# Kernel tuning notes

Measured on AMD Instinct MI355X. Metric: run time of the kernel, lower is better.

Reference implementation:

```python
import jax, jax.numpy as jnp
import numpy as np

BS, L, D, N = 4, 2048, 1024, 16

def setup_inputs() -> dict:
    key = jax.random.key(0)
    ks = jax.random.split(key, 8)
    s = 1.0 / np.sqrt(D)
    x  = jax.random.normal(ks[0], (BS, L, D), dtype=jnp.float32)
    # torch Linear params; stored transposed so y = x @ W + b
    W1 = jax.random.uniform(ks[1], (D, D), jnp.float32, -s, s)
    b1 = jax.random.uniform(ks[2], (D,),   jnp.float32, -s, s)
    W2 = jax.random.uniform(ks[3], (D, N), jnp.float32, -s, s)
    b2 = jax.random.uniform(ks[4], (N,),   jnp.float32, -s, s)
    W3 = jax.random.uniform(ks[5], (D, N), jnp.float32, -s, s)
    b3 = jax.random.uniform(ks[6], (N,),   jnp.float32, -s, s)
    A  = jax.random.normal(ks[7], (D, N),  jnp.float32) * np.sqrt(2.0 / (D + N))  # xavier
    return {"x": x, "W1": W1, "b1": b1, "W2": W2, "b2": b2, "W3": W3, "b3": b3, "A": A}

def reference(x, W1, b1, W2, b2, W3, b3, A):
    # S6 forward (non-recurrent branch).
    B = x @ W2 + b2                     # (b,l,n)
    C = x @ W3 + b3                     # (b,l,n)
    delta = jax.nn.softplus(x @ W1 + b1)  # (b,l,d)
    # dA = exp(einsum('bld,dn->bldn', delta, A)) is multiplied by an all-zero h
    # in the original forward, so it does not affect the output (dead code under DCE).
    dB = jnp.einsum('bld,bln->bldn', delta, B)   # (b,l,d,n) -- 512 MB intermediate
    h = x[..., None] * dB                         # (b,l,d,n)
    y = jnp.einsum('bln,bldn->bld', C, h)         # (b,l,d)
    return y
```

## Files before the change

kernel.cpp:

```cpp
#include <hip/hip_runtime.h>
#include <hip/hip_bf16.h>
#include <math.h>


namespace {

constexpr int Dd   = 1024;
constexpr int ROWS = 8192;

typedef __bf16 bf16x8 __attribute__((ext_vector_type(8)));
typedef float  floatx4 __attribute__((ext_vector_type(4)));

__device__ __forceinline__ float softplus_fast(float v) {
    float l = __logf(1.0f + __expf(v));
    return v > 15.0f ? v : l;
}
__device__ __forceinline__ float bf_lo(unsigned short u) {
    union { unsigned q; float f; } c; c.q = ((unsigned)u) << 16; return c.f;
}

__device__ __forceinline__ void gld_lds16(const __bf16* g, __bf16* l) {
    __builtin_amdgcn_global_load_lds(
        (const __attribute__((address_space(1))) void*)g,
        (__attribute__((address_space(3))) void*)l, 16, 0, 0);
}

__global__ __launch_bounds__(256) void w23_kernel(
    const float* __restrict__ W2, const float* __restrict__ W3,
    __bf16* __restrict__ W2t, __bf16* __restrict__ W3t)
{
    const int t  = threadIdx.x;
    const int n  = t >> 4;
    const int k0 = blockIdx.x * 64 + (t & 15) * 4;
    ushort4 a, b;
    union { __bf16 h; unsigned short u; } c;
    c.h = (__bf16)W2[(size_t)(k0 + 0) * 16 + n]; a.x = c.u;
    c.h = (__bf16)W2[(size_t)(k0 + 1) * 16 + n]; a.y = c.u;
    c.h = (__bf16)W2[(size_t)(k0 + 2) * 16 + n]; a.z = c.u;
    c.h = (__bf16)W2[(size_t)(k0 + 3) * 16 + n]; a.w = c.u;
    c.h = (__bf16)W3[(size_t)(k0 + 0) * 16 + n]; b.x = c.u;
    c.h = (__bf16)W3[(size_t)(k0 + 1) * 16 + n]; b.y = c.u;
    c.h = (__bf16)W3[(size_t)(k0 + 2) * 16 + n]; b.z = c.u;
    c.h = (__bf16)W3[(size_t)(k0 + 3) * 16 + n]; b.w = c.u;
    *(ushort4*)&W2t[(size_t)n * Dd + k0] = a;
    *(ushort4*)&W3t[(size_t)n * Dd + k0] = b;
}

__global__ __launch_bounds__(256, 4) void prep_kernel(
    const float* __restrict__ X, const float* __restrict__ W1,
    const __bf16* __restrict__ W2t, const float* __restrict__ b2,
    const __bf16* __restrict__ W3t, const float* __restrict__ b3,
    __bf16* __restrict__ Xb, __bf16* __restrict__ W1t, float* __restrict__ Sv)
{
    const int t = threadIdx.x;

    if (blockIdx.x >= 512) {
        __shared__ __bf16 tile[64][66];
        const int bidx = blockIdx.x - 512;
        const int bi = bidx >> 4, bj = bidx & 15;
        const int c = t & 63, r4 = t >> 6;
        #pragma unroll
        for (int i = 0; i < 16; ++i) {
            const int r = i * 4 + r4;
            tile[r][c] = (__bf16)W1[(size_t)(bi * 64 + r) * Dd + bj * 64 + c];
        }
        __syncthreads();
        #pragma unroll
        for (int i = 0; i < 16; ++i) {
            const int r = i * 4 + r4;
            W1t[(size_t)(bj * 64 + r) * Dd + bi * 64 + c] = tile[c][r];
        }
        return;
    }

    __shared__ float red[4][2][16][16];
    const int w = t >> 6, lane = t & 63;
    const int l15 = lane & 15, quad = lane >> 4;
    const int row0 = blockIdx.x * 16;
    const int kw = w * 256;
    const size_t xoff = (size_t)(row0 + l15) * Dd;
    const size_t woff = (size_t)l15 * Dd;

    floatx4 acc0 = {0.f, 0.f, 0.f, 0.f}, acc1 = {0.f, 0.f, 0.f, 0.f};
    #pragma unroll
    for (int ks = 0; ks < 8; ++ks) {
        const int k0 = kw + ks * 32 + quad * 8;
        const float4 xa = *(const float4*)&X[xoff + k0];
        const float4 xb = *(const float4*)&X[xoff + k0 + 4];
        bf16x8 af;
        af[0] = (__bf16)xa.x; af[1] = (__bf16)xa.y;
        af[2] = (__bf16)xa.z; af[3] = (__bf16)xa.w;
        af[4] = (__bf16)xb.x; af[5] = (__bf16)xb.y;
        af[6] = (__bf16)xb.z; af[7] = (__bf16)xb.w;
        *(bf16x8*)&Xb[xoff + k0] = af;
        const bf16x8 w2f = *(const bf16x8*)&W2t[woff + k0];
        const bf16x8 w3f = *(const bf16x8*)&W3t[woff + k0];
        acc0 = __builtin_amdgcn_mfma_f32_16x16x32_bf16(af, w2f, acc0, 0, 0, 0);
        acc1 = __builtin_amdgcn_mfma_f32_16x16x32_bf16(af, w3f, acc1, 0, 0, 0);
    }
    #pragma unroll
    for (int r = 0; r < 4; ++r) {
        red[w][0][quad * 4 + r][l15] = acc0[r];
        red[w][1][quad * 4 + r][l15] = acc1[r];
    }
    __syncthreads();
    {
        const int r = t >> 4, n = t & 15;
        float B = b2[n], C = b3[n];
        #pragma unroll
        for (int ww = 0; ww < 4; ++ww) {
            B += red[ww][0][r][n];
            C += red[ww][1][r][n];
        }
        float p = B * C;
        p += __shfl_xor(p, 1); p += __shfl_xor(p, 2);
        p += __shfl_xor(p, 4); p += __shfl_xor(p, 8);
        if (n == 0) Sv[row0 + r] = p;
    }
}

__global__ __launch_bounds__(256, 2) void gemm_kernel(
    const __bf16* __restrict__ Xb, const __bf16* __restrict__ W1t,
    const float* __restrict__ Sv, const float* __restrict__ b1,
    float* __restrict__ Y)
{
    __shared__ __attribute__((aligned(16))) __bf16 lds[32768];
    const int t = threadIdx.x, lane = t & 63;
    const int w = t >> 6, wm = w & 1, wn = w >> 1;
    const int l15 = lane & 15, quad = lane >> 4;
    const int cb = blockIdx.x & 7, rb = blockIdx.x >> 3;
    const int row0 = rb * 128, col0 = cb * 128;

    floatx4 acc[4][4] = {};

    const __bf16* gA[4]; const __bf16* gB[4];
    int dA[4], dB[4];
    #pragma unroll
    for (int i = 0; i < 4; ++i) {
        const int u = i * 256 + t;
        const int r = u >> 3;
        const int c = (u & 7) ^ (r & 7);
        gA[i] = Xb  + (size_t)(row0 + r) * Dd + c * 8;
        gB[i] = W1t + (size_t)(col0 + r) * Dd + c * 8;
        dA[i] = u * 8;
        dB[i] = 16384 + u * 8;
    }

    auto stage = [&](int buf, int k) {
        #pragma unroll
        for (int i = 0; i < 4; ++i) {
            gld_lds16(gA[i] + k, &lds[buf * 8192 + dA[i]]);
            gld_lds16(gB[i] + k, &lds[buf * 8192 + dB[i]]);
        }
    };

    auto compute = [&](int buf) {
        const __bf16* Al = &lds[buf * 8192];
        const __bf16* Bl = &lds[16384 + buf * 8192];
        #pragma unroll
        for (int ks = 0; ks < 2; ++ks) {
            const int sA = ((ks << 2) | quad) ^ (l15 & 7);
            bf16x8 af[4], bfr[4];
            #pragma unroll
            for (int mt = 0; mt < 4; ++mt)
                af[mt] = *(const bf16x8*)&Al[(wm * 64 + mt * 16 + l15) * 64 + sA * 8];
            #pragma unroll
            for (int nt = 0; nt < 4; ++nt)
                bfr[nt] = *(const bf16x8*)&Bl[(wn * 64 + nt * 16 + l15) * 64 + sA * 8];
            #pragma unroll
            for (int mt = 0; mt < 4; ++mt)
                #pragma unroll
                for (int nt = 0; nt < 4; ++nt)
                    acc[mt][nt] = __builtin_amdgcn_mfma_f32_16x16x32_bf16(
                        af[mt], bfr[nt], acc[mt][nt], 0, 0, 0);
        }
    };

    stage(0, 0);
    #pragma unroll 1
    for (int k0 = 0; k0 < Dd - 64; k0 += 64) {
        const int cur = (k0 >> 6) & 1;
        stage(cur ^ 1, k0 + 64);
        asm volatile("s_waitcnt vmcnt(8)" ::: "memory");
        __builtin_amdgcn_s_barrier();
        compute(cur);
        asm volatile("s_waitcnt lgkmcnt(0)" ::: "memory");
        __builtin_amdgcn_s_barrier();
    }
    asm volatile("s_waitcnt vmcnt(0)" ::: "memory");
    __builtin_amdgcn_s_barrier();
    compute(((Dd >> 6) - 1) & 1);

    float bias[4];
    #pragma unroll
    for (int nt = 0; nt < 4; ++nt) bias[nt] = b1[col0 + wn * 64 + nt * 16 + l15];

    #pragma unroll
    for (int mt = 0; mt < 4; ++mt) {
        #pragma unroll
        for (int rr = 0; rr < 4; ++rr) {
            const int row = row0 + wm * 64 + mt * 16 + quad * 4 + rr;
            const float sv = Sv[row];
            const unsigned short* xrow =
                (const unsigned short*)(Xb + (size_t)row * Dd + col0);
            float* yrow = Y + (size_t)row * Dd + col0;
            #pragma unroll
            for (int nt = 0; nt < 4; ++nt) {
                const int cl = wn * 64 + nt * 16 + l15;
                const float v  = acc[mt][nt][rr] + bias[nt];
                const float sp = softplus_fast(v);
                yrow[cl] = bf_lo(xrow[cl]) * sp * sv;
            }
        }
    }
}

}

extern "C" void kernel_launch(void* const* d_in, const int* in_sizes, int n_in,
                              void* d_out, int out_size, void* d_ws, size_t ws_size,
                              hipStream_t stream)
{
    const float* X  = (const float*)d_in[0];
    const float* W1 = (const float*)d_in[1];
    const float* b1 = (const float*)d_in[2];
    const float* W2 = (const float*)d_in[3];
    const float* b2 = (const float*)d_in[4];
    const float* W3 = (const float*)d_in[5];
    const float* b3 = (const float*)d_in[6];
    float* Y = (float*)d_out;

    char* ws = (char*)d_ws;
    __bf16* Xb  = (__bf16*)ws;
    __bf16* W1t = (__bf16*)(ws + 16777216);
    float*  Sv  = (float*) (ws + 16777216 + 2097152);
    __bf16* W2t = (__bf16*)(ws + 16777216 + 2097152 + 32768);
    __bf16* W3t = (__bf16*)(ws + 16777216 + 2097152 + 65536);

    hipLaunchKernelGGL(w23_kernel, dim3(16), dim3(256), 0, stream, W2, W3, W2t, W3t);
    hipLaunchKernelGGL(prep_kernel, dim3(768), dim3(256), 0, stream,
                       X, W1, W2t, b2, W3t, b3, Xb, W1t, Sv);
    hipLaunchKernelGGL(gemm_kernel, dim3((ROWS / 128) * (Dd / 128)), dim3(256), 0, stream,
                       Xb, W1t, Sv, b1, Y);
}
```

Baseline: 131.6 us.

## Restructure GEMM into 256x128 tiles with deep multi-stage LDS pipeline and ping-pong scheduling

Changes the main GEMM from 128x128 tiles with 256 threads and double buffering to 256x128 tiles with 512 threads, using a six-slot LDS ring of K=32 stages. The new schedule interleaves LDS reads, async global-to-LDS loads and MFMA bursts with barriers and setprio, aiming to hide memory latency and keep the matrix cores busy. It roughly doubles LDS use per block to about 144KB. That may limit occupancy to one block per CU, and the hand-tuned vmcnt accounting is fragile.

```diff
diff --git a/kernel.cpp b/kernel.cpp
--- a/kernel.cpp
+++ b/kernel.cpp
@@ -24,6 +24,10 @@
         (const __attribute__((address_space(1))) void*)g,
         (__attribute__((address_space(3))) void*)l, 16, 0, 0);
 }
+
+#define BAR()    asm volatile("s_barrier" ::: "memory")
+#define LGKM0()  asm volatile("s_waitcnt lgkmcnt(0)" ::: "memory")
+#define VMCNT(n) asm volatile("s_waitcnt vmcnt(" #n ")" ::: "memory")
 
 __global__ __launch_bounds__(256) void w23_kernel(
     const float* __restrict__ W2, const float* __restrict__ W3,
@@ -119,94 +123,119 @@
     }
 }
 
-__global__ __launch_bounds__(256, 2) void gemm_kernel(
+#define MF(mt, nt, a_, b_) \
+    acc[mt][nt] = __builtin_amdgcn_mfma_f32_16x16x32_bf16(a_, b_, acc[mt][nt], 0, 0, 0)
+#define MFMA8(mb) do { \
+    __builtin_amdgcn_s_setprio(1); \
+    MF(mb + 0, 0, af0, bf0); MF(mb + 0, 1, af0, bf1); \
+    MF(mb + 1, 0, af1, bf0); MF(mb + 1, 1, af1, bf1); \
+    MF(mb + 2, 0, af2, bf0); MF(mb + 2, 1, af2, bf1); \
+    MF(mb + 3, 0, af3, bf0); MF(mb + 3, 1, af3, bf1); \
+    __builtin_amdgcn_s_setprio(0); } while (0)
+
+#define TILE(B0_, B1_, NX1_, KA_, KB_, S1_, S2_, N1_, N2_) do { \
+    bf16x8 af0, af1, af2, af3, bf0, bf1; \
+     \
+    af0 = rdA(B0_, 0); af1 = rdA(B0_, 1); af2 = rdA(B0_, 2); af3 = rdA(B0_, 3); \
+    bf0 = rdB(B0_, 0); bf1 = rdB(B0_, 1); \
+    if (S1_) { stageA(NX1_, KA_); stageB(NX1_, KA_); } \
+    BAR(); LGKM0(); MFMA8(0); BAR(); \
+     \
+    af0 = rdA(B0_, 4); af1 = rdA(B0_, 5); af2 = rdA(B0_, 6); af3 = rdA(B0_, 7); \
+    BAR(); LGKM0(); MFMA8(4); VMCNT(N1_); BAR(); \
+     \
+    af0 = rdA(B1_, 0); af1 = rdA(B1_, 1); af2 = rdA(B1_, 2); af3 = rdA(B1_, 3); \
+    bf0 = rdB(B1_, 0); bf1 = rdB(B1_, 1); \
+    if (S2_) { stageA(B0_, KB_); stageB(B0_, KB_); } \
+    BAR(); LGKM0(); MFMA8(0); BAR(); \
+     \
+    af0 = rdA(B1_, 4); af1 = rdA(B1_, 5); af2 = rdA(B1_, 6); af3 = rdA(B1_, 7); \
+    BAR(); LGKM0(); MFMA8(4); VMCNT(N2_); BAR(); \
+} while (0)
+
+__global__ __launch_bounds__(512, 2) void gemm_kernel(
     const __bf16* __restrict__ Xb, const __bf16* __restrict__ W1t,
     const float* __restrict__ Sv, const float* __restrict__ b1,
     float* __restrict__ Y)
 {
-    __shared__ __attribute__((aligned(16))) __bf16 lds[32768];
+    __shared__ __attribute__((aligned(16))) __bf16 lds[73728];
     const int t = threadIdx.x, lane = t & 63;
     const int w = t >> 6, wm = w & 1, wn = w >> 1;
     const int l15 = lane & 15, quad = lane >> 4;
     const int cb = blockIdx.x & 7, rb = blockIdx.x >> 3;
-    const int row0 = rb * 128, col0 = cb * 128;
-
-    floatx4 acc[4][4] = {};
-
-    const __bf16* gA[4]; const __bf16* gB[4];
-    int dA[4], dB[4];
-    #pragma unroll
-    for (int i = 0; i < 4; ++i) {
-        const int u = i * 256 + t;
-        const int r = u >> 3;
-        const int c = (u & 7) ^ (r & 7);
-        gA[i] = Xb  + (size_t)(row0 + r) * Dd + c * 8;
-        gB[i] = W1t + (size_t)(col0 + r) * Dd + c * 8;
-        dA[i] = u * 8;
-        dB[i] = 16384 + u * 8;
-    }
-
-    auto stage = [&](int buf, int k) {
-        #pragma unroll
-        for (int i = 0; i < 4; ++i) {
-            gld_lds16(gA[i] + k, &lds[buf * 8192 + dA[i]]);
-            gld_lds16(gB[i] + k, &lds[buf * 8192 + dB[i]]);
-        }
-    };
-
-    auto compute = [&](int buf) {
-        const __bf16* Al = &lds[buf * 8192];
-        const __bf16* Bl = &lds[16384 + buf * 8192];
-        #pragma unroll
-        for (int ks = 0; ks < 2; ++ks) {
-            const int sA = ((ks << 2) | quad) ^ (l15 & 7);
-            bf16x8 af[4], bfr[4];
-            #pragma unroll
-            for (int mt = 0; mt < 4; ++mt)
-                af[mt] = *(const bf16x8*)&Al[(wm * 64 + mt * 16 + l15) * 64 + sA * 8];
-            #pragma unroll
-            for (int nt = 0; nt < 4; ++nt)
-                bfr[nt] = *(const bf16x8*)&Bl[(wn * 64 + nt * 16 + l15) * 64 + sA * 8];
-            #pragma unroll
-            for (int mt = 0; mt < 4; ++mt)
-                #pragma unroll
-                for (int nt = 0; nt < 4; ++nt)
-                    acc[mt][nt] = __builtin_amdgcn_mfma_f32_16x16x32_bf16(
-                        af[mt], bfr[nt], acc[mt][nt], 0, 0, 0);
-        }
-    };
-
-    stage(0, 0);
+    const int row0 = rb * 256, col0 = cb * 128;
+
+    floatx4 acc[8][2] = {};
+
+    const __bf16* gAs[2]; int dAs[2];
+    #pragma unroll
+    for (int i = 0; i < 2; ++i) {
+        const int d = i * 512 + t, r = d >> 2, cp = d & 3, c = cp ^ ((r >> 1) & 3);
+        gAs[i] = Xb + (size_t)(row0 + r) * Dd + c * 8;
+        dAs[i] = d * 8;
+    }
+    const __bf16* gBs; int dBs;
+    {
+        const int d = t, r = d >> 2, cp = d & 3, c = cp ^ ((r >> 1) & 3);
+        gBs = W1t + (size_t)(col0 + r) * Dd + c * 8;
+        dBs = d * 8;
+    }
+
+    auto stageA = [&](int slot, int kb) {
+        #pragma unroll
+        for (int i = 0; i < 2; ++i)
+            gld_lds16(gAs[i] + kb, &lds[slot * 8192 + dAs[i]]);
+    };
+    auto stageB = [&](int slot, int kb) {
+        gld_lds16(gBs + kb, &lds[49152 + slot * 4096 + dBs]);
+    };
+
+    const int sc  = (quad ^ ((l15 >> 1) & 3)) * 8;
+    const int aro = (wm * 128 + l15) * 32 + sc;
+    const int bro = (wn * 32 + l15) * 32 + sc;
+
+    auto rdA = [&](int slot, int mt) {
+        return *(const bf16x8*)&lds[slot * 8192 + aro + mt * 512];
+    };
+    auto rdB = [&](int slot, int nt) {
+        return *(const bf16x8*)&lds[49152 + slot * 4096 + bro + nt * 512];
+    };
+
+    stageA(0, 0);   stageB(0, 0);
+    stageA(1, 32);  stageB(1, 32);
+    stageA(2, 64);  stageB(2, 64);
+    stageA(3, 96);  stageB(3, 96);
+    stageA(4, 128); stageB(4, 128);
+    VMCNT(12); BAR();
+
+    int um3 = 0;
     #pragma unroll 1
-    for (int k0 = 0; k0 < Dd - 64; k0 += 64) {
-        const int cur = (k0 >> 6) & 1;
-        stage(cur ^ 1, k0 + 64);
-        asm volatile("s_waitcnt vmcnt(8)" ::: "memory");
-        __builtin_amdgcn_s_barrier();
-        compute(cur);
-        asm volatile("s_waitcnt lgkmcnt(0)" ::: "memory");
-        __builtin_amdgcn_s_barrier();
-    }
-    asm volatile("s_waitcnt vmcnt(0)" ::: "memory");
-    __builtin_amdgcn_s_barrier();
-    compute(((Dd >> 6) - 1) & 1);
-
-    float bias[4];
-    #pragma unroll
-    for (int nt = 0; nt < 4; ++nt) bias[nt] = b1[col0 + wn * 64 + nt * 16 + l15];
-
-    #pragma unroll
-    for (int mt = 0; mt < 4; ++mt) {
+    for (int u = 0; u <= 12; ++u) {
+        const int b0 = um3 * 2, b1v = b0 + 1;
+        const int nx1 = (um3 == 0) ? 5 : (um3 == 1) ? 1 : 3;
+        TILE(b0, b1v, nx1, (u + 2) * 64 + 32, (u + 3) * 64, true, true, 12, 12);
+        um3 = (um3 == 2) ? 0 : um3 + 1;
+    }
+    TILE(2, 3, 1, 992, 0, true,  false, 12, 9);
+    TILE(4, 5, 3, 0,   0, false, false, 6,  3);
+    TILE(0, 1, 5, 0,   0, false, false, 0,  0);
+
+    float bias[2];
+    #pragma unroll
+    for (int nt = 0; nt < 2; ++nt) bias[nt] = b1[col0 + wn * 32 + nt * 16 + l15];
+
+    #pragma unroll
+    for (int mt = 0; mt < 8; ++mt) {
         #pragma unroll
         for (int rr = 0; rr < 4; ++rr) {
-            const int row = row0 + wm * 64 + mt * 16 + quad * 4 + rr;
+            const int row = row0 + wm * 128 + mt * 16 + quad * 4 + rr;
             const float sv = Sv[row];
             const unsigned short* xrow =
                 (const unsigned short*)(Xb + (size_t)row * Dd + col0);
             float* yrow = Y + (size_t)row * Dd + col0;
             #pragma unroll
-            for (int nt = 0; nt < 4; ++nt) {
-                const int cl = wn * 64 + nt * 16 + l15;
+            for (int nt = 0; nt < 2; ++nt) {
+                const int cl = wn * 32 + nt * 16 + l15;
                 const float v  = acc[mt][nt][rr] + bias[nt];
                 const float sp = softplus_fast(v);
                 yrow[cl] = bf_lo(xrow[cl]) * sp * sv;
@@ -240,6 +269,6 @@
     hipLaunchKernelGGL(w23_kernel, dim3(16), dim3(256), 0, stream, W2, W3, W2t, W3t);
     hipLaunchKernelGGL(prep_kernel, dim3(768), dim3(256), 0, stream,
                        X, W1, W2t, b2, W3t, b3, Xb, W1t, Sv);
-    hipLaunchKernelGGL(gemm_kernel, dim3((ROWS / 128) * (Dd / 128)), dim3(256), 0, stream,
+    hipLaunchKernelGGL(gemm_kernel, dim3((ROWS / 256) * (Dd / 128)), dim3(512), 0, stream,
                        Xb, W1t, Sv, b1, Y);
 }
```

Result: slower. 136.1 us (+3.5%).
